# Optimization experiments

Measured on AMD Instinct MI355X. Metric: run time of the kernel, lower is better.

The kernel has to match this reference:

```python
import jax, jax.numpy as jnp
import numpy as np

WIN_SIZE = 256
PATCH_SIZE = [8]
CHANNEL = 32
B_CH = 256        # B_outer(8) * CHANNEL(32)
H, E = 8, 64


def _attn(q, k):
    # q, k: [B*ch, L, H, E] -> softmax scores [B*ch, H, L, L]
    scale = 1.0 / jnp.sqrt(jnp.asarray(E, q.dtype))
    scores = jnp.einsum('blhe,bshe->bhls', q, k) * scale
    return jax.nn.softmax(scores, axis=-1)  # dropout is identity in eval


def _channel_mean(a):
    # '(b reduce_b) l m n -> b l m n' mean with reduce_b=CHANNEL (channel innermost)
    bc, h, m, n = a.shape
    return a.reshape(bc // CHANNEL, CHANNEL, h, m, n).mean(axis=1)


def setup_inputs() -> dict:
    key = jax.random.key(0)
    k1, k2, k3, k4 = jax.random.split(key, 4)
    p = PATCH_SIZE[0]
    patch_num = WIN_SIZE // p
    return {
        'queries_patch_size': jax.random.normal(k1, (B_CH, patch_num, H, E), jnp.float32),
        'keys_patch_size':    jax.random.normal(k2, (B_CH, patch_num, H, E), jnp.float32),
        'queries_patch_num':  jax.random.normal(k3, (B_CH, p, H, E), jnp.float32),
        'keys_patch_num':     jax.random.normal(k4, (B_CH, p, H, E), jnp.float32),
        'patch_index': 0,
        'attn_mask': 0,
    }


def reference(queries_patch_size, keys_patch_size, queries_patch_num, keys_patch_num, patch_index, attn_mask):
    p = PATCH_SIZE[patch_index]
    rep = WIN_SIZE // p

    # patch_size branch: element-wise repeat (einops repeat) then channel mean.
    # mean over channel commutes with the repeat, so reduce first (same math,
    # avoids the 536MB intermediate the torch code materializes).
    s_ps = _channel_mean(_attn(queries_patch_size, keys_patch_size))  # [B,H,rep,rep]
    s_ps = jnp.repeat(jnp.repeat(s_ps, p, axis=2), p, axis=3)

    # patch_num branch: torch .repeat == tile, then channel mean (also commutes).
    s_pn = _channel_mean(_attn(queries_patch_num, keys_patch_num))    # [B,H,p,p]
    s_pn = jnp.tile(s_pn, (1, 1, rep, rep))

    return (s_ps, s_pn)
```

## Files before the change

### kernel.cpp

```cpp
#include <hip/hip_runtime.h>
#include <stdint.h>


__global__ __launch_bounds__(256, 4)
void scores_kernel(const float* __restrict__ qps,
                   const float* __restrict__ kps,
                   const float* __restrict__ qpn,
                   const float* __restrict__ kpn,
                   float* __restrict__ ws_ps,
                   float* __restrict__ ws_pn)
{
    __shared__ float4 tiles[2][2][32 * 17];
    const int tid  = threadIdx.x;
    const int wv   = tid >> 6;
    const int lane = tid & 63;
    const int blk  = blockIdx.x;

    if (blk < 512) {
        const int a     = blk >> 3;
        const int chunk = blk & 7;
        const int bo = a >> 3, h = a & 7;
        const int b0 = bo * 32 + chunk * 4;

        const float4* Q4 = reinterpret_cast<const float4*>(qps);
        const float4* K4 = reinterpret_cast<const float4*>(kps);

        const int r0 = tid >> 4;
        const int f  = tid & 15;

        const int myrow = wv * 8 + (lane >> 3);
        const int j     = lane & 7;

        float pa[4];
        #pragma unroll
        for (int u = 0; u < 4; ++u) pa[u] = 0.f;

        float4 gq0, gq1, gk0, gk1;
        {
            const int b = b0;
            gq0 = Q4[((b * 32 + r0) * 8 + h) * 16 + f];
            gq1 = Q4[((b * 32 + 16 + r0) * 8 + h) * 16 + f];
            gk0 = K4[((b * 32 + r0) * 8 + h) * 16 + f];
            gk1 = K4[((b * 32 + 16 + r0) * 8 + h) * 16 + f];
            tiles[0][0][r0 * 17 + f]        = gq0;
            tiles[0][0][(16 + r0) * 17 + f] = gq1;
            tiles[0][1][r0 * 17 + f]        = gk0;
            tiles[0][1][(16 + r0) * 17 + f] = gk1;
        }
        __syncthreads();

        for (int ch = 0; ch < 4; ++ch) {
            const int buf = ch & 1;

            if (ch < 3) {
                const int b = b0 + ch + 1;
                gq0 = Q4[((b * 32 + r0) * 8 + h) * 16 + f];
                gq1 = Q4[((b * 32 + 16 + r0) * 8 + h) * 16 + f];
                gk0 = K4[((b * 32 + r0) * 8 + h) * 16 + f];
                gk1 = K4[((b * 32 + 16 + r0) * 8 + h) * 16 + f];
            }

            float acc[4];
            #pragma unroll
            for (int u = 0; u < 4; ++u) acc[u] = 0.f;
            #pragma unroll
            for (int c = 0; c < 16; ++c) {
                const float4 q = tiles[buf][0][myrow * 17 + c];
                #pragma unroll
                for (int u = 0; u < 4; ++u) {
                    const float4 k = tiles[buf][1][(4 * j + u) * 17 + c];
                    acc[u] = fmaf(q.x, k.x, acc[u]);
                    acc[u] = fmaf(q.y, k.y, acc[u]);
                    acc[u] = fmaf(q.z, k.z, acc[u]);
                    acc[u] = fmaf(q.w, k.w, acc[u]);
                }
            }

            {
                float v0 = acc[0] * 0.125f, v1 = acc[1] * 0.125f;
                float v2 = acc[2] * 0.125f, v3 = acc[3] * 0.125f;
                float m = fmaxf(fmaxf(v0, v1), fmaxf(v2, v3));
                m = fmaxf(m, __shfl_xor(m, 1));
                m = fmaxf(m, __shfl_xor(m, 2));
                m = fmaxf(m, __shfl_xor(m, 4));
                float e0 = __expf(v0 - m), e1 = __expf(v1 - m);
                float e2 = __expf(v2 - m), e3 = __expf(v3 - m);
                float s = (e0 + e1) + (e2 + e3);
                s += __shfl_xor(s, 1);
                s += __shfl_xor(s, 2);
                s += __shfl_xor(s, 4);
                const float inv = 1.f / (s * 32.f);
                pa[0] += e0 * inv; pa[1] += e1 * inv;
                pa[2] += e2 * inv; pa[3] += e3 * inv;
            }

            if (ch < 3) {
                const int nb = buf ^ 1;
                tiles[nb][0][r0 * 17 + f]        = gq0;
                tiles[nb][0][(16 + r0) * 17 + f] = gq1;
                tiles[nb][1][r0 * 17 + f]        = gk0;
                tiles[nb][1][(16 + r0) * 17 + f] = gk1;
            }
            __syncthreads();
        }

        float4 o; o.x = pa[0]; o.y = pa[1]; o.z = pa[2]; o.w = pa[3];
        reinterpret_cast<float4*>(ws_ps + (a * 8 + chunk) * 1024)[myrow * 8 + j] = o;
    } else {
        float* red = reinterpret_cast<float*>(tiles);
        const int bb    = blk - 512;
        const int a2    = bb >> 3;
        const int chunk = bb & 7;
        const int bo = a2 >> 3, h = a2 & 7;
        const int b  = bo * 32 + chunk * 4 + wv;
        const int i = lane >> 3, j = lane & 7;
        const float4* qv = reinterpret_cast<const float4*>(qpn) + ((b * 8 + i) * 8 + h) * 16;
        const float4* kv = reinterpret_cast<const float4*>(kpn) + ((b * 8 + j) * 8 + h) * 16;

        float acc = 0.f;
        #pragma unroll
        for (int c = 0; c < 16; ++c) {
            float4 q = qv[c], k = kv[c];
            acc = fmaf(q.x, k.x, acc);
            acc = fmaf(q.y, k.y, acc);
            acc = fmaf(q.z, k.z, acc);
            acc = fmaf(q.w, k.w, acc);
        }
        const float s = acc * 0.125f;
        float m = s;
        m = fmaxf(m, __shfl_xor(m, 1));
        m = fmaxf(m, __shfl_xor(m, 2));
        m = fmaxf(m, __shfl_xor(m, 4));
        float e = __expf(s - m);
        float sum = e;
        sum += __shfl_xor(sum, 1);
        sum += __shfl_xor(sum, 2);
        sum += __shfl_xor(sum, 4);

        red[wv * 64 + lane] = e / (sum * 32.f);
        __syncthreads();
        if (tid < 64) {
            ws_pn[(a2 * 8 + chunk) * 64 + tid] =
                (red[0 * 64 + tid] + red[1 * 64 + tid]) +
                (red[2 * 64 + tid] + red[3 * 64 + tid]);
        }
    }
}

__global__ __launch_bounds__(256)
void reduce_kernel(const float* __restrict__ ws_ps,
                   const float* __restrict__ ws_pn,
                   float* __restrict__ ws0r,
                   float* __restrict__ ws1r)
{
    const int g = blockIdx.x * 256 + threadIdx.x;
    if (g < 65536) {
        const int a = g >> 10, c = g & 1023;
        const float* base = ws_ps + a * 8192 + c;
        float v = 0.f;
        #pragma unroll
        for (int k = 0; k < 8; ++k) v += base[k * 1024];
        ws0r[g] = v;
    } else {
        const int h = g - 65536;
        const int a = h >> 6, c = h & 63;
        const float* base = ws_pn + a * 512 + c;
        float v = 0.f;
        #pragma unroll
        for (int k = 0; k < 8; ++k) v += base[k * 64];
        ws1r[h] = v;
    }
}

__global__ __launch_bounds__(256)
void writer_kernel(const float* __restrict__ ws0r,
                   const float* __restrict__ ws1r,
                   float* __restrict__ out)
{
    const int g = blockIdx.x * 256 + threadIdx.x;
    float4* o4 = reinterpret_cast<float4*>(out);
    if (g < 1048576) {
        const int a  = g >> 14;
        const int r  = g & 16383;
        const int i  = r >> 6;
        const int j4 = r & 63;
        const float v = ws0r[a * 1024 + (i >> 3) * 32 + (j4 >> 1)];
        float4 o; o.x = v; o.y = v; o.z = v; o.w = v;
        o4[g] = o;
    } else {
        const int g2 = g - 1048576;
        const int a  = g2 >> 14;
        const int r  = g2 & 16383;
        const int i  = r >> 6;
        const int j4 = r & 63;
        o4[g] = *reinterpret_cast<const float4*>(ws1r + a * 64 + (i & 7) * 8 + 4 * (j4 & 1));
    }
}

extern "C" void kernel_launch(void* const* d_in, const int* in_sizes, int n_in,
                              void* d_out, int out_size, void* d_ws, size_t ws_size,
                              hipStream_t stream) {
    const float *qps = nullptr, *kps = nullptr, *qpn = nullptr, *kpn = nullptr;
    for (int idx = 0; idx < n_in; ++idx) {
        if (in_sizes[idx] == 256 * 32 * 8 * 64) {
            if (!qps) qps = (const float*)d_in[idx];
            else if (!kps) kps = (const float*)d_in[idx];
        } else if (in_sizes[idx] == 256 * 8 * 8 * 64) {
            if (!qpn) qpn = (const float*)d_in[idx];
            else if (!kpn) kpn = (const float*)d_in[idx];
        }
    }

    float* ws_ps = (float*)d_ws;
    float* ws_pn = ws_ps + 64 * 8 * 1024;
    float* ws0r  = ws_pn + 64 * 8 * 64;
    float* ws1r  = ws0r + 64 * 1024;

    scores_kernel<<<1024, 256, 0, stream>>>(qps, kps, qpn, kpn, ws_ps, ws_pn);
    reduce_kernel<<<272, 256, 0, stream>>>(ws_ps, ws_pn, ws0r, ws1r);
    writer_kernel<<<8192, 256, 0, stream>>>(ws0r, ws1r, (float*)d_out);
}
```

Measured before the change: 106.4 us.

## Per-wave channel scoring with LDS reduction and fold reduce into writer kernel

The scores kernel now gives each wave its own channel, loaded straight into registers and then LDS. Each lane computes a 4x4 register tile of scores, and the four waves' softmax results are summed through a swizzled LDS buffer, which replaces the serial double-buffered loop over channels. The separate reduce kernel is removed, and the writer kernel now sums the 8 chunk partials itself, saving one launch and one workspace round trip. The cost is redundant partial reads in the writer, since each partial is re-read by many output threads, plus larger LDS use and a lower occupancy hint.

New measurement: 108.6 us. +2.1%, slower.

```diff
diff --git a/kernel.cpp b/kernel.cpp
--- a/kernel.cpp
+++ b/kernel.cpp
@@ -2,7 +2,7 @@
 #include <stdint.h>
 
 
-__global__ __launch_bounds__(256, 4)
+__global__ __launch_bounds__(256, 2)
 void scores_kernel(const float* __restrict__ qps,
                    const float* __restrict__ kps,
                    const float* __restrict__ qpn,
@@ -10,7 +10,7 @@
                    float* __restrict__ ws_ps,
                    float* __restrict__ ws_pn)
 {
-    __shared__ float4 tiles[2][2][32 * 17];
+    __shared__ float4 T[4][2][32 * 17];
     const int tid  = threadIdx.x;
     const int wv   = tid >> 6;
     const int lane = tid & 63;
@@ -20,94 +20,106 @@
         const int a     = blk >> 3;
         const int chunk = blk & 7;
         const int bo = a >> 3, h = a & 7;
-        const int b0 = bo * 32 + chunk * 4;
+        const int b  = bo * 32 + chunk * 4 + wv;
 
         const float4* Q4 = reinterpret_cast<const float4*>(qps);
         const float4* K4 = reinterpret_cast<const float4*>(kps);
 
-        const int r0 = tid >> 4;
-        const int f  = tid & 15;
-
-        const int myrow = wv * 8 + (lane >> 3);
-        const int j     = lane & 7;
-
-        float pa[4];
-        #pragma unroll
-        for (int u = 0; u < 4; ++u) pa[u] = 0.f;
-
-        float4 gq0, gq1, gk0, gk1;
-        {
-            const int b = b0;
-            gq0 = Q4[((b * 32 + r0) * 8 + h) * 16 + f];
-            gq1 = Q4[((b * 32 + 16 + r0) * 8 + h) * 16 + f];
-            gk0 = K4[((b * 32 + r0) * 8 + h) * 16 + f];
-            gk1 = K4[((b * 32 + 16 + r0) * 8 + h) * 16 + f];
-            tiles[0][0][r0 * 17 + f]        = gq0;
-            tiles[0][0][(16 + r0) * 17 + f] = gq1;
-            tiles[0][1][r0 * 17 + f]        = gk0;
-            tiles[0][1][(16 + r0) * 17 + f] = gk1;
-        }
-        __syncthreads();
-
-        for (int ch = 0; ch < 4; ++ch) {
-            const int buf = ch & 1;
-
-            if (ch < 3) {
-                const int b = b0 + ch + 1;
-                gq0 = Q4[((b * 32 + r0) * 8 + h) * 16 + f];
-                gq1 = Q4[((b * 32 + 16 + r0) * 8 + h) * 16 + f];
-                gk0 = K4[((b * 32 + r0) * 8 + h) * 16 + f];
-                gk1 = K4[((b * 32 + 16 + r0) * 8 + h) * 16 + f];
-            }
-
-            float acc[4];
-            #pragma unroll
-            for (int u = 0; u < 4; ++u) acc[u] = 0.f;
-            #pragma unroll
-            for (int c = 0; c < 16; ++c) {
-                const float4 q = tiles[buf][0][myrow * 17 + c];
+        const int sr = lane >> 4;
+        const int f  = lane & 15;
+        float4 qreg[8], kreg[8];
+        #pragma unroll
+        for (int i = 0; i < 8; ++i) {
+            const int row = i * 4 + sr;
+            qreg[i] = Q4[((b * 32 + row) * 8 + h) * 16 + f];
+            kreg[i] = K4[((b * 32 + row) * 8 + h) * 16 + f];
+        }
+        #pragma unroll
+        for (int i = 0; i < 8; ++i) {
+            const int row = i * 4 + sr;
+            T[wv][0][row * 17 + f] = qreg[i];
+            T[wv][1][row * 17 + f] = kreg[i];
+        }
+
+        const int rg = lane >> 3;
+        const int cg = lane & 7;
+
+        float acc[4][4];
+        #pragma unroll
+        for (int r = 0; r < 4; ++r)
+            #pragma unroll
+            for (int u = 0; u < 4; ++u) acc[r][u] = 0.f;
+
+        #pragma unroll
+        for (int c = 0; c < 16; ++c) {
+            float4 qv[4], kv[4];
+            #pragma unroll
+            for (int r = 0; r < 4; ++r) qv[r] = T[wv][0][(rg + 8 * r) * 17 + c];
+            #pragma unroll
+            for (int u = 0; u < 4; ++u) kv[u] = T[wv][1][(cg + 8 * u) * 17 + c];
+            #pragma unroll
+            for (int r = 0; r < 4; ++r)
                 #pragma unroll
                 for (int u = 0; u < 4; ++u) {
-                    const float4 k = tiles[buf][1][(4 * j + u) * 17 + c];
-                    acc[u] = fmaf(q.x, k.x, acc[u]);
-                    acc[u] = fmaf(q.y, k.y, acc[u]);
-                    acc[u] = fmaf(q.z, k.z, acc[u]);
-                    acc[u] = fmaf(q.w, k.w, acc[u]);
+                    acc[r][u] = fmaf(qv[r].x, kv[u].x, acc[r][u]);
+                    acc[r][u] = fmaf(qv[r].y, kv[u].y, acc[r][u]);
+                    acc[r][u] = fmaf(qv[r].z, kv[u].z, acc[r][u]);
+                    acc[r][u] = fmaf(qv[r].w, kv[u].w, acc[r][u]);
                 }
+        }
+
+        #pragma unroll
+        for (int r = 0; r < 4; ++r) {
+            float v0 = acc[r][0] * 0.125f, v1 = acc[r][1] * 0.125f;
+            float v2 = acc[r][2] * 0.125f, v3 = acc[r][3] * 0.125f;
+            float m = fmaxf(fmaxf(v0, v1), fmaxf(v2, v3));
+            m = fmaxf(m, __shfl_xor(m, 1));
+            m = fmaxf(m, __shfl_xor(m, 2));
+            m = fmaxf(m, __shfl_xor(m, 4));
+            float e0 = __expf(v0 - m), e1 = __expf(v1 - m);
+            float e2 = __expf(v2 - m), e3 = __expf(v3 - m);
+            float s = (e0 + e1) + (e2 + e3);
+            s += __shfl_xor(s, 1);
+            s += __shfl_xor(s, 2);
+            s += __shfl_xor(s, 4);
+            const float inv = 1.f / (s * 32.f);
+            acc[r][0] = e0 * inv; acc[r][1] = e1 * inv;
+            acc[r][2] = e2 * inv; acc[r][3] = e3 * inv;
+        }
+
+        __syncthreads();
+        float* P = reinterpret_cast<float*>(T);
+        #pragma unroll
+        for (int r = 0; r < 4; ++r) {
+            const int row = rg + 8 * r;
+            const int sw  = (row & 3) << 3;
+            #pragma unroll
+            for (int u = 0; u < 4; ++u) {
+                const int col = cg + 8 * u;
+                P[wv * 1024 + row * 32 + (col ^ sw)] = acc[r][u];
             }
-
-            {
-                float v0 = acc[0] * 0.125f, v1 = acc[1] * 0.125f;
-                float v2 = acc[2] * 0.125f, v3 = acc[3] * 0.125f;
-                float m = fmaxf(fmaxf(v0, v1), fmaxf(v2, v3));
-                m = fmaxf(m, __shfl_xor(m, 1));
-                m = fmaxf(m, __shfl_xor(m, 2));
-                m = fmaxf(m, __shfl_xor(m, 4));
-                float e0 = __expf(v0 - m), e1 = __expf(v1 - m);
-                float e2 = __expf(v2 - m), e3 = __expf(v3 - m);
-                float s = (e0 + e1) + (e2 + e3);
-                s += __shfl_xor(s, 1);
-                s += __shfl_xor(s, 2);
-                s += __shfl_xor(s, 4);
-                const float inv = 1.f / (s * 32.f);
-                pa[0] += e0 * inv; pa[1] += e1 * inv;
-                pa[2] += e2 * inv; pa[3] += e3 * inv;
+        }
+        __syncthreads();
+
+        {
+            const int row = tid >> 3;
+            const int c0  = (tid & 7) * 4;
+            const int sw  = (row & 3) << 3;
+            float vx[4];
+            #pragma unroll
+            for (int x = 0; x < 4; ++x) {
+                const int ci = row * 32 + ((c0 + x) ^ sw);
+                float v = P[ci];
+                v += P[1024 + ci];
+                v += P[2048 + ci];
+                v += P[3072 + ci];
+                vx[x] = v;
             }
-
-            if (ch < 3) {
-                const int nb = buf ^ 1;
-                tiles[nb][0][r0 * 17 + f]        = gq0;
-                tiles[nb][0][(16 + r0) * 17 + f] = gq1;
-                tiles[nb][1][r0 * 17 + f]        = gk0;
-                tiles[nb][1][(16 + r0) * 17 + f] = gk1;
-            }
-            __syncthreads();
-        }
-
-        float4 o; o.x = pa[0]; o.y = pa[1]; o.z = pa[2]; o.w = pa[3];
-        reinterpret_cast<float4*>(ws_ps + (a * 8 + chunk) * 1024)[myrow * 8 + j] = o;
+            float4 o; o.x = vx[0]; o.y = vx[1]; o.z = vx[2]; o.w = vx[3];
+            reinterpret_cast<float4*>(ws_ps + (a * 8 + chunk) * 1024)[tid] = o;
+        }
     } else {
-        float* red = reinterpret_cast<float*>(tiles);
+        float* red = reinterpret_cast<float*>(T);
         const int bb    = blk - 512;
         const int a2    = bb >> 3;
         const int chunk = bb & 7;
@@ -148,33 +160,8 @@
 }
 
 __global__ __launch_bounds__(256)
-void reduce_kernel(const float* __restrict__ ws_ps,
+void writer_kernel(const float* __restrict__ ws_ps,
                    const float* __restrict__ ws_pn,
-                   float* __restrict__ ws0r,
-                   float* __restrict__ ws1r)
-{
-    const int g = blockIdx.x * 256 + threadIdx.x;
-    if (g < 65536) {
-        const int a = g >> 10, c = g & 1023;
-        const float* base = ws_ps + a * 8192 + c;
-        float v = 0.f;
-        #pragma unroll
-        for (int k = 0; k < 8; ++k) v += base[k * 1024];
-        ws0r[g] = v;
-    } else {
-        const int h = g - 65536;
-        const int a = h >> 6, c = h & 63;
-        const float* base = ws_pn + a * 512 + c;
-        float v = 0.f;
-        #pragma unroll
-        for (int k = 0; k < 8; ++k) v += base[k * 64];
-        ws1r[h] = v;
-    }
-}
-
-__global__ __launch_bounds__(256)
-void writer_kernel(const float* __restrict__ ws0r,
-                   const float* __restrict__ ws1r,
                    float* __restrict__ out)
 {
     const int g = blockIdx.x * 256 + threadIdx.x;
@@ -184,7 +171,10 @@
         const int r  = g & 16383;
         const int i  = r >> 6;
         const int j4 = r & 63;
-        const float v = ws0r[a * 1024 + (i >> 3) * 32 + (j4 >> 1)];
+        const float* base = ws_ps + a * 8192 + (i >> 3) * 32 + (j4 >> 1);
+        float v = 0.f;
+        #pragma unroll
+        for (int c = 0; c < 8; ++c) v += base[c * 1024];
         float4 o; o.x = v; o.y = v; o.z = v; o.w = v;
         o4[g] = o;
     } else {
@@ -193,7 +183,15 @@
         const int r  = g2 & 16383;
         const int i  = r >> 6;
         const int j4 = r & 63;
-        o4[g] = *reinterpret_cast<const float4*>(ws1r + a * 64 + (i & 7) * 8 + 4 * (j4 & 1));
+        const float4* base = reinterpret_cast<const float4*>(
+            ws_pn + a * 512 + (i & 7) * 8 + 4 * (j4 & 1));
+        float4 v; v.x = 0.f; v.y = 0.f; v.z = 0.f; v.w = 0.f;
+        #pragma unroll
+        for (int c = 0; c < 8; ++c) {
+            float4 t = base[c * 16];
+            v.x += t.x; v.y += t.y; v.z += t.z; v.w += t.w;
+        }
+        o4[g] = v;
     }
 }
 
@@ -213,10 +211,7 @@
 
     float* ws_ps = (float*)d_ws;
     float* ws_pn = ws_ps + 64 * 8 * 1024;
-    float* ws0r  = ws_pn + 64 * 8 * 64;
-    float* ws1r  = ws0r + 64 * 1024;
 
     scores_kernel<<<1024, 256, 0, stream>>>(qps, kps, qpn, kpn, ws_ps, ws_pn);
-    reduce_kernel<<<272, 256, 0, stream>>>(ws_ps, ws_pn, ws0r, ws1r);
-    writer_kernel<<<8192, 256, 0, stream>>>(ws0r, ws1r, (float*)d_out);
+    writer_kernel<<<8192, 256, 0, stream>>>(ws_ps, ws_pn, (float*)d_out);
 }
```
